# Optimization experiments

Hardware: AMD Instinct MI355X
Metric: run time of the kernel (lower is better)

The kernel has to match this reference:

```python
import jax, jax.numpy as jnp
import numpy as np

N, F, H = 22, 448, 64
LN_EPS = 1e-5


def _layernorm(h, g, b):
    mu = h.mean(axis=-1, keepdims=True)
    var = ((h - mu) ** 2).mean(axis=-1, keepdims=True)
    return (h - mu) / jnp.sqrt(var + LN_EPS) * g + b


def setup_inputs() -> dict:
    key = jax.random.key(0)
    ks = jax.random.split(key, 16)
    B = 128
    x = jax.random.normal(ks[0], (B, N, F), dtype=jnp.float32)
    s = lambda fan_in: 1.0 / np.sqrt(fan_in)
    # correlation-branch edge_weight_net: Linear(2F,64) -> ReLU -> Linear(64,1) -> Sigmoid
    cw1 = jax.random.uniform(ks[1], (2 * F, 64), jnp.float32, -s(2 * F), s(2 * F))
    cb1 = jax.random.uniform(ks[2], (64,), jnp.float32, -s(2 * F), s(2 * F))
    cw2 = jax.random.uniform(ks[3], (64, 1), jnp.float32, -s(64), s(64))
    cb2 = jax.random.uniform(ks[4], (1,), jnp.float32, -s(64), s(64))
    # semantic branch
    emb = jax.random.normal(ks[5], (N, H), dtype=jnp.float32) * 0.01
    D = 2 * H + 2 * F
    sw1 = jax.random.uniform(ks[6], (D, H), jnp.float32, -s(D), s(D))
    sb1 = jax.random.uniform(ks[7], (H,), jnp.float32, -s(D), s(D))
    ln_g = jnp.ones((H,), jnp.float32)
    ln_b = jnp.zeros((H,), jnp.float32)
    sw2 = jax.random.uniform(ks[8], (H, H // 2), jnp.float32, -s(H), s(H))
    sb2 = jax.random.uniform(ks[9], (H // 2,), jnp.float32, -s(H), s(H))
    sw3 = jax.random.uniform(ks[10], (H // 2, 1), jnp.float32, -s(H // 2), s(H // 2))
    sb3 = jax.random.uniform(ks[11], (1,), jnp.float32, -s(H // 2), s(H // 2))
    thr = jnp.asarray(0.3, jnp.float32)
    alpha_p = jnp.asarray(0.6, jnp.float32)
    return dict(x=x, cw1=cw1, cb1=cb1, cw2=cw2, cb2=cb2, emb=emb,
                sw1=sw1, sb1=sb1, ln_g=ln_g, ln_b=ln_b,
                sw2=sw2, sb2=sb2, sw3=sw3, sb3=sb3,
                thr=thr, alpha_p=alpha_p)


def reference(x, cw1, cb1, cw2, cb2, emb, sw1, sb1, ln_g, ln_b,
              sw2, sb2, sw3, sb3, thr, alpha_p):
    B, n, f = x.shape
    eye = jnp.eye(n, dtype=x.dtype)[None]

    # ---- Correlation graph ----
    xc = x - x.mean(axis=-1, keepdims=True)
    std = jnp.std(x, axis=-1, ddof=1, keepdims=True) + 1e-8  # torch std is unbiased
    xn = xc / std
    corr = jnp.abs(jnp.einsum('bif,bjf->bij', xn, xn) / f)
    # pairwise edge features (B,N,N,2F)
    xi = jnp.broadcast_to(x[:, :, None, :], (B, n, n, f))
    xj = jnp.broadcast_to(x[:, None, :, :], (B, n, n, f))
    ef = jnp.concatenate([xi, xj], axis=-1)
    h = jax.nn.relu(ef @ cw1 + cb1)
    w_corr = jax.nn.sigmoid((h @ cw2 + cb2)[..., 0])
    g_corr = corr * w_corr + eye

    # ---- Semantic graph ----
    ei = jnp.broadcast_to(emb[None, :, None, :], (B, n, n, H))
    ej = jnp.broadcast_to(emb[None, None, :, :], (B, n, n, H))
    sf = jnp.concatenate([ei, ej, xi, xj], axis=-1)  # (B,N,N,2H+2F)
    h1 = jax.nn.relu(_layernorm(sf @ sw1 + sb1, ln_g, ln_b))
    h2 = jax.nn.relu(h1 @ sw2 + sb2)
    w_sem = jax.nn.sigmoid((h2 @ sw3 + sb3)[..., 0])  # (B,N,N)
    # original loop fills only i<j and mirrors; diagonal stays 0
    upper = jnp.triu(w_sem, k=1)
    adj = upper + jnp.swapaxes(upper, 1, 2)
    t = jax.nn.sigmoid(thr)
    adj = jnp.where(adj > t, adj, jnp.zeros_like(adj))
    g_sem = adj + eye

    # ---- Learned fusion ----
    alpha = jax.nn.sigmoid(alpha_p)
    return alpha * g_corr + (1.0 - alpha) * g_sem
```

## Files before the change

kernel.cpp:

```cpp
#include <hip/hip_runtime.h>
#include <math.h>

namespace {
constexpr int kN = 22;
constexpr int kF = 448;
constexpr int kNP = 484;
constexpr int kXStr = 452;
constexpr int kSm1 = kN * kXStr + 2 * kN;
constexpr int kAStr = 36;
constexpr int kBStr = 68;
constexpr int kPStr = 68;
constexpr int kTStr = 66;

__device__ __forceinline__ void map_slot(int s, int& i, int& j) {
    if (s < 231) {
        int rem = s, i0 = 0;
        while (rem >= 21 - i0) { rem -= 21 - i0; ++i0; }
        i = i0; j = i0 + 1 + rem;
    } else {
        i = j = s - 231;
    }
}
}

__global__ __launch_bounds__(256) void hgc_k1(
    const float* __restrict__ x,
    const float* __restrict__ cw1, const float* __restrict__ cb1,
    const float* __restrict__ emb,
    const float* __restrict__ sw1, const float* __restrict__ sb1,
    float* __restrict__ C, float* __restrict__ g,
    int M, int Mtiles, int nGemm)
{
    __shared__ __align__(16) float sm[kSm1];
    const int tid = threadIdx.x;

    if ((int)blockIdx.x < nGemm) {
        float* As = sm;
        float* Bs = sm + 64 * kAStr;
        const int bm = blockIdx.x % Mtiles;
        const int bn = blockIdx.x / Mtiles;
        const int m0 = bm * 32;

        const float* Wsrc =
            (bn == 0) ? cw1 :
            (bn == 1) ? cw1 + 448 * 64 :
            (bn == 2) ? sw1 + 128 * 64 :
                        sw1 + 576 * 64;

        const int kg   = tid >> 7;
        const int t128 = tid & 127;
        const int mg = t128 >> 4;
        const int ng = t128 & 15;
        float4 acc[4];
        #pragma unroll
        for (int i = 0; i < 4; ++i) acc[i] = float4{0, 0, 0, 0};

        float4 rA[2], rB[4];

        auto preMain = [&](int k0) {
            #pragma unroll
            for (int p = 0; p < 2; ++p) {
                const int idx = tid + p * 256;
                const int row = idx >> 4, kq = idx & 15;
                int m = m0 + row; if (m >= M) m = M - 1;
                rA[p] = *(const float4*)&x[(size_t)m * kF + k0 + kq * 4];
            }
            #pragma unroll
            for (int p = 0; p < 4; ++p) {
                const int idx = tid + p * 256;
                const int k = idx >> 4, nq = idx & 15;
                rB[p] = *(const float4*)&Wsrc[(size_t)(k0 + k) * 64 + nq * 4];
            }
        };
        auto preEmb = [&]() {
            const float* W2 = sw1 + (bn == 2 ? 0 : 64) * 64;
            #pragma unroll
            for (int p = 0; p < 2; ++p) {
                const int idx = tid + p * 256;
                const int row = idx >> 4, kq = idx & 15;
                const int r = (m0 + row) % kN;
                rA[p] = *(const float4*)&emb[(size_t)r * 64 + kq * 4];
            }
            #pragma unroll
            for (int p = 0; p < 4; ++p) {
                const int idx = tid + p * 256;
                const int k = idx >> 4, nq = idx & 15;
                rB[p] = *(const float4*)&W2[(size_t)k * 64 + nq * 4];
            }
        };
        auto commit = [&]() {
            #pragma unroll
            for (int p = 0; p < 2; ++p) {
                const int idx = tid + p * 256;
                const int row = idx >> 4, kq = idx & 15;
                As[(kq * 4 + 0) * kAStr + row] = rA[p].x;
                As[(kq * 4 + 1) * kAStr + row] = rA[p].y;
                As[(kq * 4 + 2) * kAStr + row] = rA[p].z;
                As[(kq * 4 + 3) * kAStr + row] = rA[p].w;
            }
            #pragma unroll
            for (int p = 0; p < 4; ++p) {
                const int idx = tid + p * 256;
                const int k = idx >> 4, nq = idx & 15;
                *(float4*)&Bs[k * kBStr + nq * 4] = rB[p];
            }
        };
        auto compute = [&]() {
            #pragma unroll 8
            for (int kk = 0; kk < 32; ++kk) {
                const int k = kg * 32 + kk;
                const float4 a4 = *(const float4*)&As[k * kAStr + mg * 4];
                const float4 b4 = *(const float4*)&Bs[k * kBStr + ng * 4];
                acc[0].x = fmaf(a4.x, b4.x, acc[0].x); acc[0].y = fmaf(a4.x, b4.y, acc[0].y);
                acc[0].z = fmaf(a4.x, b4.z, acc[0].z); acc[0].w = fmaf(a4.x, b4.w, acc[0].w);
                acc[1].x = fmaf(a4.y, b4.x, acc[1].x); acc[1].y = fmaf(a4.y, b4.y, acc[1].y);
                acc[1].z = fmaf(a4.y, b4.z, acc[1].z); acc[1].w = fmaf(a4.y, b4.w, acc[1].w);
                acc[2].x = fmaf(a4.z, b4.x, acc[2].x); acc[2].y = fmaf(a4.z, b4.y, acc[2].y);
                acc[2].z = fmaf(a4.z, b4.z, acc[2].z); acc[2].w = fmaf(a4.z, b4.w, acc[2].w);
                acc[3].x = fmaf(a4.w, b4.x, acc[3].x); acc[3].y = fmaf(a4.w, b4.y, acc[3].y);
                acc[3].z = fmaf(a4.w, b4.z, acc[3].z); acc[3].w = fmaf(a4.w, b4.w, acc[3].w);
            }
        };

        preMain(0);
        commit();
        __syncthreads();
        for (int c = 0; c < 7; ++c) {
            if (c < 6) preMain((c + 1) * 64);
            else if (bn >= 2) preEmb();
            compute();
            __syncthreads();
            if (c < 6 || bn >= 2) {
                commit();
                __syncthreads();
            }
        }
        if (bn >= 2) compute();

        __syncthreads();
        float* red = sm;
        if (kg == 1) {
            #pragma unroll
            for (int i = 0; i < 4; ++i)
                *(float4*)&red[i * 512 + t128 * 4] = acc[i];
        }
        __syncthreads();
        if (kg == 0) {
            float4 bias = {0, 0, 0, 0};
            if (bn == 0)      bias = *(const float4*)&cb1[ng * 4];
            else if (bn == 2) bias = *(const float4*)&sb1[ng * 4];
            #pragma unroll
            for (int i = 0; i < 4; ++i) {
                const float4 r = *(const float4*)&red[i * 512 + t128 * 4];
                const int m = m0 + mg * 4 + i;
                if (m < M) {
                    float4 o;
                    o.x = acc[i].x + r.x + bias.x; o.y = acc[i].y + r.y + bias.y;
                    o.z = acc[i].z + r.z + bias.z; o.w = acc[i].w + r.w + bias.w;
                    *(float4*)&C[(size_t)m * 256 + bn * 64 + ng * 4] = o;
                }
            }
        }
    } else {
        float* smu = sm + kN * kXStr;
        float* sis = smu + kN;
        const int cb = blockIdx.x - nGemm;
        const int b = cb >> 1;
        const int r0 = (cb & 1) * 11;

        const float4* xb4 = (const float4*)(x + (size_t)b * (kN * kF));
        for (int idx = tid; idx < kN * kF / 4; idx += 256) {
            const float4 v = xb4[idx];
            const int r = idx / 112;
            const int k = (idx - r * 112) * 4;
            float* d = sm + r * kXStr + k;
            d[0] = v.x; d[1] = v.y; d[2] = v.z; d[3] = v.w;
        }
        __syncthreads();

        {
            const int wid = tid >> 6, lane = tid & 63;
            for (int r = wid; r < kN; r += 4) {
                const float* row = sm + r * kXStr;
                float s = 0.f;
                #pragma unroll
                for (int c = 0; c < 7; ++c) s += row[c * 64 + lane];
                #pragma unroll
                for (int o = 32; o; o >>= 1) s += __shfl_xor(s, o, 64);
                const float mean = s * (1.f / 448.f);
                float ss = 0.f;
                #pragma unroll
                for (int c = 0; c < 7; ++c) { const float d = row[c * 64 + lane] - mean; ss = fmaf(d, d, ss); }
                #pragma unroll
                for (int o = 32; o; o >>= 1) ss += __shfl_xor(ss, o, 64);
                if (lane == 0) {
                    smu[r] = mean;
                    sis[r] = 1.f / (sqrtf(ss * (1.f / 447.f)) + 1e-8f);
                }
            }
        }
        __syncthreads();

        for (int p = tid; p < 11 * kN; p += 256) {
            const int pi = p / 22;
            const int i = r0 + pi, j = p - pi * 22;
            const float4* ri = (const float4*)(sm + i * kXStr);
            const float4* rj = (const float4*)(sm + j * kXStr);
            float dot = 0.f;
            for (int q = 0; q < 112; ++q) {
                const float4 a = ri[q], bq = rj[q];
                dot = fmaf(a.x, bq.x, dot); dot = fmaf(a.y, bq.y, dot);
                dot = fmaf(a.z, bq.z, dot); dot = fmaf(a.w, bq.w, dot);
            }
            const float c = (dot - 448.f * smu[i] * smu[j]) * sis[i] * sis[j] * (1.f / 448.f);
            g[(size_t)b * kNP + i * 22 + j] = fabsf(c);
        }
    }
}

__global__ __launch_bounds__(256) void hgc_k2(
    const float* __restrict__ C, const float* __restrict__ g,
    const float* __restrict__ cw2, const float* __restrict__ cb2,
    const float* __restrict__ sw2, const float* __restrict__ sb2,
    const float* __restrict__ sw3, const float* __restrict__ sb3,
    const float* __restrict__ ln_g, const float* __restrict__ ln_b,
    const float* __restrict__ thr, const float* __restrict__ alpha_p,
    float* __restrict__ out)
{
    __shared__ __align__(16) float sp[4 * kN * kPStr];
    __shared__ float sg[kNP];
    __shared__ __align__(16) float sw2s[2048];
    __shared__ float scw2[64], slng[64], slnb[64], ssw3[32], ssb2[32];
    __shared__ float szc[128];
    __shared__ __align__(16) float vbT[64 * kTStr];

    const int tid = threadIdx.x;
    const int b   = blockIdx.x >> 2;
    const int pb  = blockIdx.x & 3;

    #pragma unroll
    for (int a = 0; a < 4; ++a) {
        float* dst = sp + a * kN * kPStr;
        for (int idx = tid; idx < 352; idx += 256) {
            const int r = idx >> 4, kq = idx & 15;
            const float4 v = *(const float4*)&C[((size_t)(b * 22 + r)) * 256 + a * 64 + kq * 4];
            *(float4*)&dst[r * kPStr + kq * 4] = v;
        }
    }
    for (int idx = tid; idx < kNP; idx += 256) sg[idx] = g[(size_t)b * kNP + idx];
    {
        const float4* s4 = (const float4*)sw2;
        for (int idx = tid; idx < 512; idx += 256)
            *((float4*)(sw2s + idx * 4)) = s4[idx];
    }
    if (tid < 64)       { scw2[tid] = cw2[tid]; slng[tid] = ln_g[tid]; slnb[tid] = ln_b[tid]; }
    else if (tid < 96)  { ssw3[tid - 64] = sw3[tid - 64]; }
    else if (tid < 128) { ssb2[tid - 96] = sb2[tid - 96]; }
    __syncthreads();

    const float* sa1 = sp;
    const float* sa2 = sp + kN * kPStr;
    const float* su1 = sp + 2 * kN * kPStr;
    const float* su2 = sp + 3 * kN * kPStr;

    {
        const int sl = tid >> 2, t4 = tid & 3;
        const int s_ = pb * 64 + sl;
        const int s = (s_ < 253) ? s_ : 252;
        int i, j; map_slot(s, i, j);

        float zc1 = 0.f, zc2 = 0.f;
        {
            const float* a1i = sa1 + i * kPStr + t4 * 16;
            const float* a2j = sa2 + j * kPStr + t4 * 16;
            const float* a1j = sa1 + j * kPStr + t4 * 16;
            const float* a2i = sa2 + i * kPStr + t4 * 16;
            #pragma unroll
            for (int c4 = 0; c4 < 4; ++c4) {
                const float4 p = *(const float4*)(a1i + c4 * 4);
                const float4 q = *(const float4*)(a2j + c4 * 4);
                const float4 r = *(const float4*)(a1j + c4 * 4);
                const float4 t = *(const float4*)(a2i + c4 * 4);
                const float4 w = *(const float4*)(scw2 + t4 * 16 + c4 * 4);
                zc1 = fmaf(fmaxf(p.x + q.x, 0.f), w.x, zc1);
                zc1 = fmaf(fmaxf(p.y + q.y, 0.f), w.y, zc1);
                zc1 = fmaf(fmaxf(p.z + q.z, 0.f), w.z, zc1);
                zc1 = fmaf(fmaxf(p.w + q.w, 0.f), w.w, zc1);
                zc2 = fmaf(fmaxf(r.x + t.x, 0.f), w.x, zc2);
                zc2 = fmaf(fmaxf(r.y + t.y, 0.f), w.y, zc2);
                zc2 = fmaf(fmaxf(r.z + t.z, 0.f), w.z, zc2);
                zc2 = fmaf(fmaxf(r.w + t.w, 0.f), w.w, zc2);
            }
            zc1 += __shfl_xor(zc1, 1, 64); zc1 += __shfl_xor(zc1, 2, 64);
            zc2 += __shfl_xor(zc2, 1, 64); zc2 += __shfl_xor(zc2, 2, 64);
            if (t4 == 0) { szc[sl * 2] = zc1; szc[sl * 2 + 1] = zc2; }
        }

        float raw[16];
        float s1 = 0.f;
        {
            const float* pu1 = su1 + i * kPStr + t4 * 16;
            const float* pu2 = su2 + j * kPStr + t4 * 16;
            #pragma unroll
            for (int c4 = 0; c4 < 4; ++c4) {
                const float4 a = *(const float4*)(pu1 + c4 * 4);
                const float4 e = *(const float4*)(pu2 + c4 * 4);
                raw[c4*4+0] = a.x + e.x; raw[c4*4+1] = a.y + e.y;
                raw[c4*4+2] = a.z + e.z; raw[c4*4+3] = a.w + e.w;
                s1 += raw[c4*4+0] + raw[c4*4+1] + raw[c4*4+2] + raw[c4*4+3];
            }
        }
        s1 += __shfl_xor(s1, 1, 64); s1 += __shfl_xor(s1, 2, 64);
        const float mean = s1 * (1.f / 64.f);
        float s2 = 0.f;
        #pragma unroll
        for (int c = 0; c < 16; ++c) { const float d = raw[c] - mean; s2 = fmaf(d, d, s2); }
        s2 += __shfl_xor(s2, 1, 64); s2 += __shfl_xor(s2, 2, 64);
        const float rstd = rsqrtf(s2 * (1.f / 64.f) + 1e-5f);
        #pragma unroll
        for (int c = 0; c < 16; ++c) {
            const int k = t4 * 16 + c;
            vbT[k * kTStr + sl] = fmaxf(fmaf((raw[c] - mean) * rstd, slng[k], slnb[k]), 0.f);
        }
    }
    __syncthreads();

    {
        const int w = tid >> 6, l = tid & 63;
        const int sg8 = l >> 3, cq = l & 7;
        const int sl0 = w * 16 + sg8 * 2;
        float4 a0 = {0,0,0,0}, a1 = {0,0,0,0};
        for (int k = 0; k < 64; ++k) {
            const float4 w4 = *(const float4*)&sw2s[k * 32 + cq * 4];
            const float2 v2 = *(const float2*)&vbT[k * kTStr + sl0];
            a0.x = fmaf(v2.x, w4.x, a0.x); a0.y = fmaf(v2.x, w4.y, a0.y);
            a0.z = fmaf(v2.x, w4.z, a0.z); a0.w = fmaf(v2.x, w4.w, a0.w);
            a1.x = fmaf(v2.y, w4.x, a1.x); a1.y = fmaf(v2.y, w4.y, a1.y);
            a1.z = fmaf(v2.y, w4.z, a1.z); a1.w = fmaf(v2.y, w4.w, a1.w);
        }
        const int o0 = cq * 4;
        float z0, z1;
        z0  = fmaxf(a0.x + ssb2[o0+0], 0.f) * ssw3[o0+0];
        z0 += fmaxf(a0.y + ssb2[o0+1], 0.f) * ssw3[o0+1];
        z0 += fmaxf(a0.z + ssb2[o0+2], 0.f) * ssw3[o0+2];
        z0 += fmaxf(a0.w + ssb2[o0+3], 0.f) * ssw3[o0+3];
        z1  = fmaxf(a1.x + ssb2[o0+0], 0.f) * ssw3[o0+0];
        z1 += fmaxf(a1.y + ssb2[o0+1], 0.f) * ssw3[o0+1];
        z1 += fmaxf(a1.z + ssb2[o0+2], 0.f) * ssw3[o0+2];
        z1 += fmaxf(a1.w + ssb2[o0+3], 0.f) * ssw3[o0+3];
        z0 += __shfl_xor(z0, 1, 64); z0 += __shfl_xor(z0, 2, 64); z0 += __shfl_xor(z0, 4, 64);
        z1 += __shfl_xor(z1, 1, 64); z1 += __shfl_xor(z1, 2, 64); z1 += __shfl_xor(z1, 4, 64);

        if (cq == 0) {
            const float alpha = 1.f / (1.f + __expf(-alpha_p[0]));
            const float cb2s  = cb2[0];
            #pragma unroll
            for (int e = 0; e < 2; ++e) {
                const int sl = sl0 + e;
                const float z = e ? z1 : z0;
                const int s_ = pb * 64 + sl;
                if (s_ < 253) {
                    int i, j; map_slot(s_, i, j);
                    const float zc1 = szc[sl * 2];
                    const float zc2 = szc[sl * 2 + 1];
                    const float wc1 = 1.f / (1.f + __expf(-(zc1 + cb2s)));
                    float gsem;
                    if (i == j) {
                        gsem = 1.f;
                    } else {
                        const float wsem = 1.f / (1.f + expf(-(z + sb3[0])));
                        const float tt   = 1.f / (1.f + expf(-thr[0]));
                        gsem = (wsem > tt) ? wsem : 0.f;
                    }
                    const float gc1 = fmaf(sg[i * 22 + j], wc1, (i == j) ? 1.f : 0.f);
                    out[(size_t)b * kNP + i * 22 + j] = fmaf(alpha, gc1, (1.f - alpha) * gsem);
                    if (i != j) {
                        const float wc2 = 1.f / (1.f + __expf(-(zc2 + cb2s)));
                        const float gc2 = sg[j * 22 + i] * wc2;
                        out[(size_t)b * kNP + j * 22 + i] = fmaf(alpha, gc2, (1.f - alpha) * gsem);
                    }
                }
            }
        }
    }
}

extern "C" void kernel_launch(void* const* d_in, const int* in_sizes, int n_in,
                              void* d_out, int out_size, void* d_ws, size_t ws_size,
                              hipStream_t stream)
{
    (void)n_in; (void)out_size; (void)ws_size;
    const float* x     = (const float*)d_in[0];
    const float* cw1   = (const float*)d_in[1];
    const float* cb1   = (const float*)d_in[2];
    const float* cw2   = (const float*)d_in[3];
    const float* cb2   = (const float*)d_in[4];
    const float* emb   = (const float*)d_in[5];
    const float* sw1   = (const float*)d_in[6];
    const float* sb1   = (const float*)d_in[7];
    const float* ln_g  = (const float*)d_in[8];
    const float* ln_b  = (const float*)d_in[9];
    const float* sw2   = (const float*)d_in[10];
    const float* sb2   = (const float*)d_in[11];
    const float* sw3   = (const float*)d_in[12];
    const float* sb3   = (const float*)d_in[13];
    const float* thr   = (const float*)d_in[14];
    const float* alpha = (const float*)d_in[15];
    float* out = (float*)d_out;
    float* ws  = (float*)d_ws;

    const int B = in_sizes[0] / (kN * kF);
    const int M = kN * B;
    const int Mtiles = (M + 31) / 32;
    const int nGemm = Mtiles * 4;

    float* C = ws;
    float* g = ws + (size_t)M * 256;

    hipLaunchKernelGGL(hgc_k1, dim3(nGemm + 2 * B), dim3(256), 0, stream,
                       x, cw1, cb1, emb, sw1, sb1, C, g, M, Mtiles, nGemm);
    hipLaunchKernelGGL(hgc_k2, dim3(4 * B), dim3(256), 0, stream,
                       C, g, cw2, cb2, sw2, sb2, sw3, sb3, ln_g, ln_b, thr, alpha, out);
}
```

Before: 128.9 us.

## Split GEMM, correlation and pair-MLP work into smaller blocks for more parallelism

The projection GEMM now uses 32-column output tiles, doubling the block count. Each thread computes a 2x2 micro-tile over the full K=64 slice, which removes the split-K shared-memory reduction. The correlation blocks are split four ways per batch instead of two, and the second kernel handles 32 pair slots per block instead of 64, so the grid doubles there too. This aims to fill the GPU's many CUs at B=128. The cost is lower per-thread arithmetic intensity, more redundant loads of x and weights per batch, and more per-block setup.

```diff
diff --git a/kernel.cpp b/kernel.cpp
--- a/kernel.cpp
+++ b/kernel.cpp
@@ -8,9 +8,9 @@
 constexpr int kXStr = 452;
 constexpr int kSm1 = kN * kXStr + 2 * kN;
 constexpr int kAStr = 36;
-constexpr int kBStr = 68;
+constexpr int kBStr = 36;
 constexpr int kPStr = 68;
-constexpr int kTStr = 66;
+constexpr int kTStr = 34;
 
 __device__ __forceinline__ void map_slot(int s, int& i, int& j) {
     if (s < 231) {
@@ -40,22 +40,20 @@
         const int bm = blockIdx.x % Mtiles;
         const int bn = blockIdx.x / Mtiles;
         const int m0 = bm * 32;
+        const int half = bn & 1;
+        const int grp  = bn >> 1;
 
         const float* Wsrc =
-            (bn == 0) ? cw1 :
-            (bn == 1) ? cw1 + 448 * 64 :
-            (bn == 2) ? sw1 + 128 * 64 :
-                        sw1 + 576 * 64;
-
-        const int kg   = tid >> 7;
-        const int t128 = tid & 127;
-        const int mg = t128 >> 4;
-        const int ng = t128 & 15;
-        float4 acc[4];
-        #pragma unroll
-        for (int i = 0; i < 4; ++i) acc[i] = float4{0, 0, 0, 0};
-
-        float4 rA[2], rB[4];
+            (grp == 0) ? cw1 + half * 32 :
+            (grp == 1) ? cw1 + 448 * 64 + half * 32 :
+            (grp == 2) ? sw1 + 128 * 64 + half * 32 :
+                         sw1 + 576 * 64 + half * 32;
+
+        const int tm = tid >> 4;
+        const int tn = tid & 15;
+        float a00 = 0.f, a01 = 0.f, a10 = 0.f, a11 = 0.f;
+
+        float4 rA[2], rB[2];
 
         auto preMain = [&](int k0) {
             #pragma unroll
@@ -66,14 +64,14 @@
                 rA[p] = *(const float4*)&x[(size_t)m * kF + k0 + kq * 4];
             }
             #pragma unroll
-            for (int p = 0; p < 4; ++p) {
-                const int idx = tid + p * 256;
-                const int k = idx >> 4, nq = idx & 15;
+            for (int p = 0; p < 2; ++p) {
+                const int idx = tid + p * 256;
+                const int k = idx >> 3, nq = idx & 7;
                 rB[p] = *(const float4*)&Wsrc[(size_t)(k0 + k) * 64 + nq * 4];
             }
         };
         auto preEmb = [&]() {
-            const float* W2 = sw1 + (bn == 2 ? 0 : 64) * 64;
+            const float* W2 = sw1 + (grp == 2 ? 0 : 64) * 64 + half * 32;
             #pragma unroll
             for (int p = 0; p < 2; ++p) {
                 const int idx = tid + p * 256;
@@ -82,9 +80,9 @@
                 rA[p] = *(const float4*)&emb[(size_t)r * 64 + kq * 4];
             }
             #pragma unroll
-            for (int p = 0; p < 4; ++p) {
-                const int idx = tid + p * 256;
-                const int k = idx >> 4, nq = idx & 15;
+            for (int p = 0; p < 2; ++p) {
+                const int idx = tid + p * 256;
+                const int k = idx >> 3, nq = idx & 7;
                 rB[p] = *(const float4*)&W2[(size_t)k * 64 + nq * 4];
             }
         };
@@ -99,26 +97,19 @@
                 As[(kq * 4 + 3) * kAStr + row] = rA[p].w;
             }
             #pragma unroll
-            for (int p = 0; p < 4; ++p) {
-                const int idx = tid + p * 256;
-                const int k = idx >> 4, nq = idx & 15;
+            for (int p = 0; p < 2; ++p) {
+                const int idx = tid + p * 256;
+                const int k = idx >> 3, nq = idx & 7;
                 *(float4*)&Bs[k * kBStr + nq * 4] = rB[p];
             }
         };
         auto compute = [&]() {
             #pragma unroll 8
-            for (int kk = 0; kk < 32; ++kk) {
-                const int k = kg * 32 + kk;
-                const float4 a4 = *(const float4*)&As[k * kAStr + mg * 4];
-                const float4 b4 = *(const float4*)&Bs[k * kBStr + ng * 4];
-                acc[0].x = fmaf(a4.x, b4.x, acc[0].x); acc[0].y = fmaf(a4.x, b4.y, acc[0].y);
-                acc[0].z = fmaf(a4.x, b4.z, acc[0].z); acc[0].w = fmaf(a4.x, b4.w, acc[0].w);
-                acc[1].x = fmaf(a4.y, b4.x, acc[1].x); acc[1].y = fmaf(a4.y, b4.y, acc[1].y);
-                acc[1].z = fmaf(a4.y, b4.z, acc[1].z); acc[1].w = fmaf(a4.y, b4.w, acc[1].w);
-                acc[2].x = fmaf(a4.z, b4.x, acc[2].x); acc[2].y = fmaf(a4.z, b4.y, acc[2].y);
-                acc[2].z = fmaf(a4.z, b4.z, acc[2].z); acc[2].w = fmaf(a4.z, b4.w, acc[2].w);
-                acc[3].x = fmaf(a4.w, b4.x, acc[3].x); acc[3].y = fmaf(a4.w, b4.y, acc[3].y);
-                acc[3].z = fmaf(a4.w, b4.z, acc[3].z); acc[3].w = fmaf(a4.w, b4.w, acc[3].w);
+            for (int k = 0; k < 64; ++k) {
+                const float2 a2 = *(const float2*)&As[k * kAStr + tm * 2];
+                const float2 b2 = *(const float2*)&Bs[k * kBStr + tn * 2];
+                a00 = fmaf(a2.x, b2.x, a00); a01 = fmaf(a2.x, b2.y, a01);
+                a10 = fmaf(a2.y, b2.x, a10); a11 = fmaf(a2.y, b2.y, a11);
             }
         };
 
@@ -127,46 +118,39 @@
         __syncthreads();
         for (int c = 0; c < 7; ++c) {
             if (c < 6) preMain((c + 1) * 64);
-            else if (bn >= 2) preEmb();
+            else if (grp >= 2) preEmb();
             compute();
             __syncthreads();
-            if (c < 6 || bn >= 2) {
+            if (c < 6 || grp >= 2) {
                 commit();
                 __syncthreads();
             }
         }
-        if (bn >= 2) compute();
-
-        __syncthreads();
-        float* red = sm;
-        if (kg == 1) {
-            #pragma unroll
-            for (int i = 0; i < 4; ++i)
-                *(float4*)&red[i * 512 + t128 * 4] = acc[i];
-        }
-        __syncthreads();
-        if (kg == 0) {
-            float4 bias = {0, 0, 0, 0};
-            if (bn == 0)      bias = *(const float4*)&cb1[ng * 4];
-            else if (bn == 2) bias = *(const float4*)&sb1[ng * 4];
-            #pragma unroll
-            for (int i = 0; i < 4; ++i) {
-                const float4 r = *(const float4*)&red[i * 512 + t128 * 4];
-                const int m = m0 + mg * 4 + i;
-                if (m < M) {
-                    float4 o;
-                    o.x = acc[i].x + r.x + bias.x; o.y = acc[i].y + r.y + bias.y;
-                    o.z = acc[i].z + r.z + bias.z; o.w = acc[i].w + r.w + bias.w;
-                    *(float4*)&C[(size_t)m * 256 + bn * 64 + ng * 4] = o;
-                }
+        if (grp >= 2) compute();
+
+        float b0 = 0.f, b1 = 0.f;
+        if (grp == 0)      { b0 = cb1[half * 32 + tn * 2]; b1 = cb1[half * 32 + tn * 2 + 1]; }
+        else if (grp == 2) { b0 = sb1[half * 32 + tn * 2]; b1 = sb1[half * 32 + tn * 2 + 1]; }
+        const int colg = bn * 32 + tn * 2;
+        {
+            const int m = m0 + tm * 2;
+            if (m < M) {
+                float2 o0; o0.x = a00 + b0; o0.y = a01 + b1;
+                *(float2*)&C[(size_t)m * 256 + colg] = o0;
+            }
+            if (m + 1 < M) {
+                float2 o1; o1.x = a10 + b0; o1.y = a11 + b1;
+                *(float2*)&C[(size_t)(m + 1) * 256 + colg] = o1;
             }
         }
     } else {
         float* smu = sm + kN * kXStr;
         float* sis = smu + kN;
         const int cb = blockIdx.x - nGemm;
-        const int b = cb >> 1;
-        const int r0 = (cb & 1) * 11;
+        const int b = cb >> 2;
+        const int qb = cb & 3;
+        const int r0 = qb * 6;
+        const int nr = (qb < 3) ? 6 : 4;
 
         const float4* xb4 = (const float4*)(x + (size_t)b * (kN * kF));
         for (int idx = tid; idx < kN * kF / 4; idx += 256) {
@@ -201,7 +185,7 @@
         }
         __syncthreads();
 
-        for (int p = tid; p < 11 * kN; p += 256) {
+        for (int p = tid; p < nr * kN; p += 256) {
             const int pi = p / 22;
             const int i = r0 + pi, j = p - pi * 22;
             const float4* ri = (const float4*)(sm + i * kXStr);
@@ -231,12 +215,12 @@
     __shared__ float sg[kNP];
     __shared__ __align__(16) float sw2s[2048];
     __shared__ float scw2[64], slng[64], slnb[64], ssw3[32], ssb2[32];
-    __shared__ float szc[128];
+    __shared__ float szc[64];
     __shared__ __align__(16) float vbT[64 * kTStr];
 
     const int tid = threadIdx.x;
-    const int b   = blockIdx.x >> 2;
-    const int pb  = blockIdx.x & 3;
+    const int b   = blockIdx.x >> 3;
+    const int pb  = blockIdx.x & 7;
 
     #pragma unroll
     for (int a = 0; a < 4; ++a) {
@@ -264,24 +248,24 @@
     const float* su2 = sp + 3 * kN * kPStr;
 
     {
-        const int sl = tid >> 2, t4 = tid & 3;
-        const int s_ = pb * 64 + sl;
+        const int sl = tid >> 3, t8 = tid & 7;
+        const int s_ = pb * 32 + sl;
         const int s = (s_ < 253) ? s_ : 252;
         int i, j; map_slot(s, i, j);
 
         float zc1 = 0.f, zc2 = 0.f;
         {
-            const float* a1i = sa1 + i * kPStr + t4 * 16;
-            const float* a2j = sa2 + j * kPStr + t4 * 16;
-            const float* a1j = sa1 + j * kPStr + t4 * 16;
-            const float* a2i = sa2 + i * kPStr + t4 * 16;
-            #pragma unroll
-            for (int c4 = 0; c4 < 4; ++c4) {
+            const float* a1i = sa1 + i * kPStr + t8 * 8;
+            const float* a2j = sa2 + j * kPStr + t8 * 8;
+            const float* a1j = sa1 + j * kPStr + t8 * 8;
+            const float* a2i = sa2 + i * kPStr + t8 * 8;
+            #pragma unroll
+            for (int c4 = 0; c4 < 2; ++c4) {
                 const float4 p = *(const float4*)(a1i + c4 * 4);
                 const float4 q = *(const float4*)(a2j + c4 * 4);
                 const float4 r = *(const float4*)(a1j + c4 * 4);
                 const float4 t = *(const float4*)(a2i + c4 * 4);
-                const float4 w = *(const float4*)(scw2 + t4 * 16 + c4 * 4);
+                const float4 w = *(const float4*)(scw2 + t8 * 8 + c4 * 4);
                 zc1 = fmaf(fmaxf(p.x + q.x, 0.f), w.x, zc1);
                 zc1 = fmaf(fmaxf(p.y + q.y, 0.f), w.y, zc1);
                 zc1 = fmaf(fmaxf(p.z + q.z, 0.f), w.z, zc1);
@@ -291,18 +275,18 @@
                 zc2 = fmaf(fmaxf(r.z + t.z, 0.f), w.z, zc2);
                 zc2 = fmaf(fmaxf(r.w + t.w, 0.f), w.w, zc2);
             }
-            zc1 += __shfl_xor(zc1, 1, 64); zc1 += __shfl_xor(zc1, 2, 64);
-            zc2 += __shfl_xor(zc2, 1, 64); zc2 += __shfl_xor(zc2, 2, 64);
-            if (t4 == 0) { szc[sl * 2] = zc1; szc[sl * 2 + 1] = zc2; }
-        }
-
-        float raw[16];
+            zc1 += __shfl_xor(zc1, 1, 64); zc1 += __shfl_xor(zc1, 2, 64); zc1 += __shfl_xor(zc1, 4, 64);
+            zc2 += __shfl_xor(zc2, 1, 64); zc2 += __shfl_xor(zc2, 2, 64); zc2 += __shfl_xor(zc2, 4, 64);
+            if (t8 == 0) { szc[sl * 2] = zc1; szc[sl * 2 + 1] = zc2; }
+        }
+
+        float raw[8];
         float s1 = 0.f;
         {
-            const float* pu1 = su1 + i * kPStr + t4 * 16;
-            const float* pu2 = su2 + j * kPStr + t4 * 16;
-            #pragma unroll
-            for (int c4 = 0; c4 < 4; ++c4) {
+            const float* pu1 = su1 + i * kPStr + t8 * 8;
+            const float* pu2 = su2 + j * kPStr + t8 * 8;
+            #pragma unroll
+            for (int c4 = 0; c4 < 2; ++c4) {
                 const float4 a = *(const float4*)(pu1 + c4 * 4);
                 const float4 e = *(const float4*)(pu2 + c4 * 4);
                 raw[c4*4+0] = a.x + e.x; raw[c4*4+1] = a.y + e.y;
@@ -310,16 +294,16 @@
                 s1 += raw[c4*4+0] + raw[c4*4+1] + raw[c4*4+2] + raw[c4*4+3];
             }
         }
-        s1 += __shfl_xor(s1, 1, 64); s1 += __shfl_xor(s1, 2, 64);
+        s1 += __shfl_xor(s1, 1, 64); s1 += __shfl_xor(s1, 2, 64); s1 += __shfl_xor(s1, 4, 64);
         const float mean = s1 * (1.f / 64.f);
         float s2 = 0.f;
         #pragma unroll
-        for (int c = 0; c < 16; ++c) { const float d = raw[c] - mean; s2 = fmaf(d, d, s2); }
-        s2 += __shfl_xor(s2, 1, 64); s2 += __shfl_xor(s2, 2, 64);
+        for (int c = 0; c < 8; ++c) { const float d = raw[c] - mean; s2 = fmaf(d, d, s2); }
+        s2 += __shfl_xor(s2, 1, 64); s2 += __shfl_xor(s2, 2, 64); s2 += __shfl_xor(s2, 4, 64);
         const float rstd = rsqrtf(s2 * (1.f / 64.f) + 1e-5f);
         #pragma unroll
-        for (int c = 0; c < 16; ++c) {
-            const int k = t4 * 16 + c;
+        for (int c = 0; c < 8; ++c) {
+            const int k = t8 * 8 + c;
             vbT[k * kTStr + sl] = fmaxf(fmaf((raw[c] - mean) * rstd, slng[k], slnb[k]), 0.f);
         }
     }
@@ -328,57 +312,45 @@
     {
         const int w = tid >> 6, l = tid & 63;
         const int sg8 = l >> 3, cq = l & 7;
-        const int sl0 = w * 16 + sg8 * 2;
-        float4 a0 = {0,0,0,0}, a1 = {0,0,0,0};
+        const int sl = w * 8 + sg8;
+        float4 a = {0, 0, 0, 0};
         for (int k = 0; k < 64; ++k) {
             const float4 w4 = *(const float4*)&sw2s[k * 32 + cq * 4];
-            const float2 v2 = *(const float2*)&vbT[k * kTStr + sl0];
-            a0.x = fmaf(v2.x, w4.x, a0.x); a0.y = fmaf(v2.x, w4.y, a0.y);
-            a0.z = fmaf(v2.x, w4.z, a0.z); a0.w = fmaf(v2.x, w4.w, a0.w);
-            a1.x = fmaf(v2.y, w4.x, a1.x); a1.y = fmaf(v2.y, w4.y, a1.y);
-            a1.z = fmaf(v2.y, w4.z, a1.z); a1.w = fmaf(v2.y, w4.w, a1.w);
+            const float v = vbT[k * kTStr + sl];
+            a.x = fmaf(v, w4.x, a.x); a.y = fmaf(v, w4.y, a.y);
+            a.z = fmaf(v, w4.z, a.z); a.w = fmaf(v, w4.w, a.w);
         }
         const int o0 = cq * 4;
-        float z0, z1;
-        z0  = fmaxf(a0.x + ssb2[o0+0], 0.f) * ssw3[o0+0];
-        z0 += fmaxf(a0.y + ssb2[o0+1], 0.f) * ssw3[o0+1];
-        z0 += fmaxf(a0.z + ssb2[o0+2], 0.f) * ssw3[o0+2];
-        z0 += fmaxf(a0.w + ssb2[o0+3], 0.f) * ssw3[o0+3];
-        z1  = fmaxf(a1.x + ssb2[o0+0], 0.f) * ssw3[o0+0];
-        z1 += fmaxf(a1.y + ssb2[o0+1], 0.f) * ssw3[o0+1];
-        z1 += fmaxf(a1.z + ssb2[o0+2], 0.f) * ssw3[o0+2];
-        z1 += fmaxf(a1.w + ssb2[o0+3], 0.f) * ssw3[o0+3];
-        z0 += __shfl_xor(z0, 1, 64); z0 += __shfl_xor(z0, 2, 64); z0 += __shfl_xor(z0, 4, 64);
-        z1 += __shfl_xor(z1, 1, 64); z1 += __shfl_xor(z1, 2, 64); z1 += __shfl_xor(z1, 4, 64);
+        float z;
+        z  = fmaxf(a.x + ssb2[o0+0], 0.f) * ssw3[o0+0];
+        z += fmaxf(a.y + ssb2[o0+1], 0.f) * ssw3[o0+1];
+        z += fmaxf(a.z + ssb2[o0+2], 0.f) * ssw3[o0+2];
+        z += fmaxf(a.w + ssb2[o0+3], 0.f) * ssw3[o0+3];
+        z += __shfl_xor(z, 1, 64); z += __shfl_xor(z, 2, 64); z += __shfl_xor(z, 4, 64);
 
         if (cq == 0) {
-            const float alpha = 1.f / (1.f + __expf(-alpha_p[0]));
-            const float cb2s  = cb2[0];
-            #pragma unroll
-            for (int e = 0; e < 2; ++e) {
-                const int sl = sl0 + e;
-                const float z = e ? z1 : z0;
-                const int s_ = pb * 64 + sl;
-                if (s_ < 253) {
-                    int i, j; map_slot(s_, i, j);
-                    const float zc1 = szc[sl * 2];
-                    const float zc2 = szc[sl * 2 + 1];
-                    const float wc1 = 1.f / (1.f + __expf(-(zc1 + cb2s)));
-                    float gsem;
-                    if (i == j) {
-                        gsem = 1.f;
-                    } else {
-                        const float wsem = 1.f / (1.f + expf(-(z + sb3[0])));
-                        const float tt   = 1.f / (1.f + expf(-thr[0]));
-                        gsem = (wsem > tt) ? wsem : 0.f;
-                    }
-                    const float gc1 = fmaf(sg[i * 22 + j], wc1, (i == j) ? 1.f : 0.f);
-                    out[(size_t)b * kNP + i * 22 + j] = fmaf(alpha, gc1, (1.f - alpha) * gsem);
-                    if (i != j) {
-                        const float wc2 = 1.f / (1.f + __expf(-(zc2 + cb2s)));
-                        const float gc2 = sg[j * 22 + i] * wc2;
-                        out[(size_t)b * kNP + j * 22 + i] = fmaf(alpha, gc2, (1.f - alpha) * gsem);
-                    }
+            const int s_ = pb * 32 + sl;
+            if (s_ < 253) {
+                int i, j; map_slot(s_, i, j);
+                const float alpha = 1.f / (1.f + __expf(-alpha_p[0]));
+                const float cb2s  = cb2[0];
+                const float zc1 = szc[sl * 2];
+                const float zc2 = szc[sl * 2 + 1];
+                const float wc1 = 1.f / (1.f + __expf(-(zc1 + cb2s)));
+                float gsem;
+                if (i == j) {
+                    gsem = 1.f;
+                } else {
+                    const float wsem = 1.f / (1.f + expf(-(z + sb3[0])));
+                    const float tt   = 1.f / (1.f + expf(-thr[0]));
+                    gsem = (wsem > tt) ? wsem : 0.f;
+                }
+                const float gc1 = fmaf(sg[i * 22 + j], wc1, (i == j) ? 1.f : 0.f);
+                out[(size_t)b * kNP + i * 22 + j] = fmaf(alpha, gc1, (1.f - alpha) * gsem);
+                if (i != j) {
+                    const float wc2 = 1.f / (1.f + __expf(-(zc2 + cb2s)));
+                    const float gc2 = sg[j * 22 + i] * wc2;
+                    out[(size_t)b * kNP + j * 22 + i] = fmaf(alpha, gc2, (1.f - alpha) * gsem);
                 }
             }
         }
@@ -412,13 +384,13 @@
     const int B = in_sizes[0] / (kN * kF);
     const int M = kN * B;
     const int Mtiles = (M + 31) / 32;
-    const int nGemm = Mtiles * 4;
+    const int nGemm = Mtiles * 8;
 
     float* C = ws;
     float* g = ws + (size_t)M * 256;
 
-    hipLaunchKernelGGL(hgc_k1, dim3(nGemm + 2 * B), dim3(256), 0, stream,
+    hipLaunchKernelGGL(hgc_k1, dim3(nGemm + 4 * B), dim3(256), 0, stream,
                        x, cw1, cb1, emb, sw1, sb1, C, g, M, Mtiles, nGemm);
-    hipLaunchKernelGGL(hgc_k2, dim3(4 * B), dim3(256), 0, stream,
+    hipLaunchKernelGGL(hgc_k2, dim3(8 * B), dim3(256), 0, stream,
                        C, g, cw2, cb2, sw2, sb2, sw3, sb3, ln_g, ln_b, thr, alpha, out);
 }
```

Result: slower. 143.1 us (+11.0%).
